# Performance work log

Hardware: AMD Instinct MI355X
Metric: run time of the kernel (lower is better)

## Reference

```python
import jax, jax.numpy as jnp
import numpy as np

F_DIM = 256; H = 4; LAT = 256; BOT = 128
B = 64; NPG = 180; N = B * NPG; E = N * 16; HF = H * F_DIM
NEG_SLOPE = 0.2  # PyG GATConv default LeakyReLU slope


def _gat(x, src, dst, W, att_s, att_d, bias):
    # PyG GATConv (concat=True): h = x W, per-edge score LeakyReLU(a_s[src]+a_d[dst]),
    # softmax over incoming edges of each dst, weighted sum, concat heads, + bias.
    h = (x @ W).reshape(N, H, F_DIM)
    a_s = jnp.einsum('nhc,hc->nh', h, att_s)
    a_d = jnp.einsum('nhc,hc->nh', h, att_d)
    e = jax.nn.leaky_relu(a_s[src] + a_d[dst], NEG_SLOPE)          # [E+N, H]
    m = jax.ops.segment_max(e, dst, num_segments=N)                # stable softmax per dst
    p = jnp.exp(e - m[dst])
    s = jax.ops.segment_sum(p, dst, num_segments=N)
    alpha = p / (s[dst] + 1e-16)
    out = jax.ops.segment_sum(alpha[:, :, None] * h[src], dst, num_segments=N)
    return out.reshape(N, HF) + bias


def setup_inputs() -> dict:
    key = jax.random.key(0)
    ks = jax.random.split(key, 40)
    def rn(i, shape, scale):
        return jax.random.normal(ks[i], shape, jnp.float32) * jnp.float32(scale)
    inp = {}
    inp['z'] = jax.random.normal(ks[0], (B, LAT), jnp.float32)
    inp['condition'] = jax.random.normal(ks[1], (B, BOT), jnp.float32)
    dst = jax.random.randint(ks[2], (E,), 0, N)
    off = jax.random.randint(ks[3], (E,), 1, NPG)
    src = (dst + off) % N  # no self-loops by construction (PyG adds them itself)
    inp['edge_index'] = jnp.stack([src, dst]).astype(jnp.int32)
    inp['batch'] = jnp.repeat(jnp.arange(B, dtype=jnp.int32), NPG)
    def lin(i, fin, fout):
        s = 1.0 / np.sqrt(fin)
        return rn(i, (fin, fout), s), rn(i + 1, (fout,), s)
    inp['W_init'], inp['b_init'] = lin(4, LAT + BOT, F_DIM)
    inp['W1'] = rn(6, (F_DIM + 180, HF), 1.0 / np.sqrt(F_DIM + 180))
    inp['as1'] = rn(7, (H, F_DIM), 0.1); inp['ad1'] = rn(8, (H, F_DIM), 0.1)
    inp['b1'] = rn(9, (HF,), 0.1)
    inp['W2'] = rn(10, (HF, HF), 1.0 / np.sqrt(HF))
    inp['as2'] = rn(11, (H, F_DIM), 0.1); inp['ad2'] = rn(12, (H, F_DIM), 0.1)
    inp['b2'] = rn(13, (HF,), 0.1)
    inp['W3'] = rn(14, (HF, HF), 1.0 / np.sqrt(HF))
    inp['as3'] = rn(15, (H, F_DIM), 0.1); inp['ad3'] = rn(16, (H, F_DIM), 0.1)
    inp['b3'] = rn(17, (HF,), 0.1)
    inp['Wp'], inp['bp'] = lin(18, HF, F_DIM)
    inp['Wfp'], inp['bfp'] = lin(20, F_DIM, 2)
    inp['Ws'], inp['bs'] = lin(22, HF, F_DIM)
    inp['Wfs'], inp['bfs'] = lin(24, F_DIM, 2)
    inp['Wt'], inp['bt'] = lin(26, HF, F_DIM)
    inp['Wft'], inp['bft'] = lin(28, F_DIM, 1)
    return inp


def reference(z, condition, edge_index, batch, W_init, b_init,
              W1, as1, ad1, b1, W2, as2, ad2, b2, W3, as3, ad3, b3,
              Wp, bp, Wfp, bfp, Ws, bs, Wfs, bfs, Wt, bt, Wft, bft):
    zc = jnp.concatenate([z, condition], axis=1) @ W_init + b_init  # [B, F]
    x = zc[batch]                                                    # [N, F]
    # node order within each (sorted) batch segment -> one-hot(180)
    start = jnp.searchsorted(batch, jnp.arange(B, dtype=batch.dtype))
    order = jnp.arange(N) - start[batch]
    pos = jax.nn.one_hot(order, 180, dtype=x.dtype)
    x = jax.nn.relu(jnp.concatenate([x, pos], axis=1))               # [N, F+180]
    # add self loops (PyG GATConv default add_self_loops=True)
    loops = jnp.arange(N, dtype=edge_index.dtype)
    src = jnp.concatenate([edge_index[0], loops])
    dst = jnp.concatenate([edge_index[1], loops])
    x = jax.nn.relu(_gat(x, src, dst, W1, as1, ad1, b1))
    x = jax.nn.relu(_gat(x, src, dst, W2, as2, ad2, b2))
    x = jax.nn.relu(_gat(x, src, dst, W3, as3, ad3, b3))
    out_pos = jax.nn.relu(x @ Wp + bp) @ Wfp + bfp     # [N, 2]
    out_size = jax.nn.relu(x @ Ws + bs) @ Wfs + bfs    # [N, 2]
    out_theta = jax.nn.relu(x @ Wt + bt) @ Wft + bft   # [N, 1]
    return out_pos, out_size, out_theta
```

## Files before the change

### kernel.cpp

```cpp
#include <hip/hip_runtime.h>
#include <hip/hip_bf16.h>

#define NODES 11520
#define EDGES 184320
#define NB    64
#define NPG   180
#define CAP   64

typedef __bf16 bf16x8 __attribute__((ext_vector_type(8)));
typedef __bf16 bf16x4 __attribute__((ext_vector_type(4)));
typedef float  f32x4  __attribute__((ext_vector_type(4)));

__global__ __launch_bounds__(256) void k_init(
    const float* __restrict__ z, const float* __restrict__ cond,
    const float* __restrict__ Wi, const float* __restrict__ bi,
    const float* __restrict__ W1, float* __restrict__ Y1)
{
    __shared__ float xr[384];
    __shared__ float zr[256];
    const int b = blockIdx.x, t = threadIdx.x;
    xr[t] = z[b * 256 + t];
    if (t < 128) xr[256 + t] = cond[b * 128 + t];
    __syncthreads();
    float acc = bi[t];
#pragma unroll 4
    for (int k = 0; k < 384; ++k) acc = fmaf(xr[k], Wi[k * 256 + t], acc);
    zr[t] = fmaxf(acc, 0.f);
    __syncthreads();
    float a0 = 0, a1 = 0, a2 = 0, a3 = 0;
#pragma unroll 4
    for (int k = 0; k < 256; ++k) {
        const float x = zr[k];
        const float* w = W1 + (size_t)k * 1024 + t;
        a0 = fmaf(x, w[0],   a0);
        a1 = fmaf(x, w[256], a1);
        a2 = fmaf(x, w[512], a2);
        a3 = fmaf(x, w[768], a3);
    }
    float* y = Y1 + (size_t)b * 1024 + t;
    y[0] = a0; y[256] = a1; y[512] = a2; y[768] = a3;
}

__global__ __launch_bounds__(256) void k_h1(
    const float* __restrict__ Y1, const float* __restrict__ W1,
    const float* __restrict__ atts, const float* __restrict__ attd,
    __bf16* __restrict__ hb, float* __restrict__ asb, float* __restrict__ adb)
{
    const int n = blockIdx.x, t = threadIdx.x;
    const int g = n / NPG, o = n - g * NPG;
    const float4 y = *(const float4*)(Y1 + (size_t)g * 1024 + 4 * t);
    const float4 w = *(const float4*)(W1 + (size_t)(256 + o) * 1024 + 4 * t);
    const float4 h = {y.x + w.x, y.y + w.y, y.z + w.z, y.w + w.w};
    bf16x4 hv = {(__bf16)h.x, (__bf16)h.y, (__bf16)h.z, (__bf16)h.w};
    *(bf16x4*)(hb + (size_t)n * 1024 + 4 * t) = hv;
    const int head = t >> 6, c0 = (t & 63) * 4;
    const float4 s4 = *(const float4*)(atts + head * 256 + c0);
    const float4 d4 = *(const float4*)(attd + head * 256 + c0);
    float ps = h.x * s4.x + h.y * s4.y + h.z * s4.z + h.w * s4.w;
    float pd = h.x * d4.x + h.y * d4.y + h.z * d4.z + h.w * d4.w;
    for (int off = 32; off; off >>= 1) {
        ps += __shfl_xor(ps, off, 64);
        pd += __shfl_xor(pd, off, 64);
    }
    if ((t & 63) == 0) { asb[n * 4 + head] = ps; adb[n * 4 + head] = pd; }
}

__global__ __launch_bounds__(256) void k_hist(
    const int* __restrict__ ei, int* __restrict__ counts,
    int* __restrict__ bucket)
{
    const int e = blockIdx.x * 256 + threadIdx.x;
    if (e >= EDGES) return;
    const int s = ei[e], d = ei[EDGES + e];
    const int pos = atomicAdd(&counts[d], 1);
    if (pos < CAP) bucket[(size_t)d * CAP + pos] = s;
}

__global__ __launch_bounds__(256) void k_agg(
    const __bf16* __restrict__ hb, const float* __restrict__ asb,
    const float* __restrict__ adb, const int* __restrict__ counts,
    const int* __restrict__ bucket, const float* __restrict__ bias,
    __bf16* __restrict__ xout)
{
    const int l = blockIdx.x;
    const int n = (l & 7) * (NODES / 8) + (l >> 3);
    const int t = threadIdx.x;
    __shared__ float sc[CAP + 1][4];
    __shared__ int   ssrc[CAP + 1];
    __shared__ float sinv[4];
    const int deg = min(counts[n], CAP);
    const int ne  = deg + 1;
    if (t < deg)       ssrc[t] = bucket[(size_t)n * CAP + t];
    else if (t == deg) ssrc[t] = n;
    __syncthreads();
    if (t < ne) {
        const int s = ssrc[t];
        const float4 as4 = *(const float4*)(asb + (size_t)s * 4);
        const float4 ad4 = *(const float4*)(adb + (size_t)n * 4);
        const float v0 = as4.x + ad4.x, v1 = as4.y + ad4.y;
        const float v2 = as4.z + ad4.z, v3 = as4.w + ad4.w;
        sc[t][0] = v0 > 0.f ? v0 : 0.2f * v0;
        sc[t][1] = v1 > 0.f ? v1 : 0.2f * v1;
        sc[t][2] = v2 > 0.f ? v2 : 0.2f * v2;
        sc[t][3] = v3 > 0.f ? v3 : 0.2f * v3;
    }
    __syncthreads();
    const int wv = t >> 6, ln = t & 63;
    {
        float m = -1e30f;
        for (int k = ln; k < ne; k += 64) m = fmaxf(m, sc[k][wv]);
        for (int off = 32; off; off >>= 1) m = fmaxf(m, __shfl_xor(m, off, 64));
        float s = 0.f;
        for (int k = ln; k < ne; k += 64) {
            const float p = __expf(sc[k][wv] - m);
            sc[k][wv] = p;
            s += p;
        }
        for (int off = 32; off; off >>= 1) s += __shfl_xor(s, off, 64);
        if (ln == 0) sinv[wv] = 1.f / (s + 1e-16f);
    }
    __syncthreads();
    const int j0 = t * 4;
    const float inv = sinv[wv];
    float a0 = 0, a1 = 0, a2 = 0, a3 = 0;
    int k = 0;
    for (; k + 4 <= ne; k += 4) {
        float al[4]; bf16x4 hv[4];
#pragma unroll
        for (int u = 0; u < 4; ++u) {
            al[u] = sc[k + u][wv] * inv;
            hv[u] = *(const bf16x4*)(hb + (size_t)ssrc[k + u] * 1024 + j0);
        }
#pragma unroll
        for (int u = 0; u < 4; ++u) {
            a0 = fmaf(al[u], (float)hv[u][0], a0);
            a1 = fmaf(al[u], (float)hv[u][1], a1);
            a2 = fmaf(al[u], (float)hv[u][2], a2);
            a3 = fmaf(al[u], (float)hv[u][3], a3);
        }
    }
    for (; k < ne; ++k) {
        const float al = sc[k][wv] * inv;
        const bf16x4 hv = *(const bf16x4*)(hb + (size_t)ssrc[k] * 1024 + j0);
        a0 = fmaf(al, (float)hv[0], a0);
        a1 = fmaf(al, (float)hv[1], a1);
        a2 = fmaf(al, (float)hv[2], a2);
        a3 = fmaf(al, (float)hv[3], a3);
    }
    const float4 b4 = *(const float4*)(bias + j0);
    bf16x4 o = {(__bf16)fmaxf(a0 + b4.x, 0.f), (__bf16)fmaxf(a1 + b4.y, 0.f),
                (__bf16)fmaxf(a2 + b4.z, 0.f), (__bf16)fmaxf(a3 + b4.w, 0.f)};
    *(bf16x4*)(xout + (size_t)n * 1024 + j0) = o;
}

__global__ __launch_bounds__(256) void k_transW(
    const float* __restrict__ W2, const float* __restrict__ W3,
    __bf16* __restrict__ W2t, __bf16* __restrict__ W3t)
{
    const float* W = blockIdx.z ? W3 : W2;
    __bf16* WT = blockIdx.z ? W3t : W2t;
    __shared__ float t[32][33];
    const int n0 = blockIdx.x * 32, k0 = blockIdx.y * 32;
    const int tx = threadIdx.x & 31, ty = threadIdx.x >> 5;
#pragma unroll
    for (int i = 0; i < 32; i += 8)
        t[ty + i][tx] = W[(size_t)(k0 + ty + i) * 1024 + n0 + tx];
    __syncthreads();
#pragma unroll
    for (int i = 0; i < 32; i += 8)
        WT[(size_t)(n0 + ty + i) * 1024 + k0 + tx] = (__bf16)t[tx][ty + i];
}

__global__ __launch_bounds__(256) void k_transH(
    const float* __restrict__ Wp, const float* __restrict__ Ws,
    const float* __restrict__ Wt, __bf16* __restrict__ WHt,
    const float* __restrict__ bp, const float* __restrict__ bs,
    const float* __restrict__ bt, float* __restrict__ bc)
{
    if (blockIdx.x == 8) {
        if (blockIdx.y == 0) {
            const int t = blockIdx.z * 256 + threadIdx.x;
            const float v = blockIdx.z == 0 ? bp[threadIdx.x]
                          : blockIdx.z == 1 ? bs[threadIdx.x] : bt[threadIdx.x];
            bc[t] = v;
        }
        return;
    }
    const float* W = blockIdx.z == 0 ? Wp : blockIdx.z == 1 ? Ws : Wt;
    __bf16* WT = WHt + (size_t)blockIdx.z * 256 * 1024;
    __shared__ float t[32][33];
    const int n0 = blockIdx.x * 32, k0 = blockIdx.y * 32;
    const int tx = threadIdx.x & 31, ty = threadIdx.x >> 5;
#pragma unroll
    for (int i = 0; i < 32; i += 8)
        t[ty + i][tx] = W[(size_t)(k0 + ty + i) * 256 + n0 + tx];
    __syncthreads();
#pragma unroll
    for (int i = 0; i < 32; i += 8)
        WT[(size_t)(n0 + ty + i) * 1024 + k0 + tx] = (__bf16)t[tx][ty + i];
}

__global__ __launch_bounds__(256) void gemm_bf16_h(
    const __bf16* __restrict__ A,
    const __bf16* __restrict__ BT,
    __bf16* __restrict__ Cb,
    const float* __restrict__ atts, const float* __restrict__ attd,
    float* __restrict__ asb, float* __restrict__ adb,
    int M, int N, int K)
{
    const int lb = blockIdx.x;
    const int g = lb & 7, idx = lb >> 3;
    const int bx = idx & 7;
    const int by = (idx >> 3) * 8 + g;
    if (by * 128 >= M) return;
    const int m0 = by * 128, n0 = bx * 128;

    __shared__ __bf16 As[128 * 32];
    __shared__ __bf16 Bs[128 * 32];
    const int tid = threadIdx.x;
    const int w = tid >> 6, l = tid & 63;
    const int lr = l >> 2;
    const int lk = (l & 3) * 8;
    const int quad = l >> 4, r16 = l & 15;
    const int wm = (w >> 1) * 64, wn = (w & 1) * 64;

    f32x4 acc[4][4];
#pragma unroll
    for (int i = 0; i < 4; ++i)
#pragma unroll
        for (int j = 0; j < 4; ++j)
            acc[i][j] = (f32x4){0.f, 0.f, 0.f, 0.f};

    for (int k0 = 0; k0 < K; k0 += 32) {
#pragma unroll
        for (int cc = 0; cc < 2; ++cc) {
            const int c = 2 * w + cc;
            const int row = c * 16 + lr;
            __builtin_amdgcn_global_load_lds(
                (const __attribute__((address_space(1))) void*)
                    (A + (size_t)(m0 + row) * K + k0 + lk),
                (__attribute__((address_space(3))) void*)(As + c * 512),
                16, 0, 0);
            __builtin_amdgcn_global_load_lds(
                (const __attribute__((address_space(1))) void*)
                    (BT + (size_t)(n0 + row) * K + k0 + lk),
                (__attribute__((address_space(3))) void*)(Bs + c * 512),
                16, 0, 0);
        }
        __syncthreads();
        bf16x8 af[4], bfr[4];
#pragma unroll
        for (int i = 0; i < 4; ++i)
            af[i] = *(const bf16x8*)(As + (wm + i * 16 + r16) * 32 + quad * 8);
#pragma unroll
        for (int j = 0; j < 4; ++j)
            bfr[j] = *(const bf16x8*)(Bs + (wn + j * 16 + r16) * 32 + quad * 8);
#pragma unroll
        for (int i = 0; i < 4; ++i)
#pragma unroll
            for (int j = 0; j < 4; ++j)
                acc[i][j] = __builtin_amdgcn_mfma_f32_16x16x32_bf16(
                    af[i], bfr[j], acc[i][j], 0, 0, 0);
        __syncthreads();
    }
    const int head = (n0 + wn) >> 8;
    const float* Sa = atts + head * 256;
    const float* Da = attd + head * 256;
#pragma unroll
    for (int i = 0; i < 4; ++i) {
#pragma unroll
        for (int r = 0; r < 4; ++r) {
            const int mg = m0 + wm + i * 16 + quad * 4 + r;
            float ps = 0.f, pd = 0.f;
#pragma unroll
            for (int j = 0; j < 4; ++j) {
                const int ng = n0 + wn + j * 16 + r16;
                const float v = acc[i][j][r];
                const int cl = ng & 255;
                ps = fmaf(v, Sa[cl], ps);
                pd = fmaf(v, Da[cl], pd);
                Cb[(size_t)mg * N + ng] = (__bf16)v;
            }
            for (int off = 8; off; off >>= 1) {
                ps += __shfl_xor(ps, off, 64);
                pd += __shfl_xor(pd, off, 64);
            }
            if (r16 == 0) {
                atomicAdd(&asb[mg * 4 + head], ps);
                atomicAdd(&adb[mg * 4 + head], pd);
            }
        }
    }
}

__global__ __launch_bounds__(256) void gemm_bf16_f32(
    const __bf16* __restrict__ A, const __bf16* __restrict__ BT,
    float* __restrict__ C, const float* __restrict__ bias,
    int M, int N, int K)
{
    const int lb = blockIdx.x;
    const int g = lb & 7, idx = lb >> 3;
    const int bx = idx % 6;
    const int by = (idx / 6) * 8 + g;
    if (by * 128 >= M) return;
    const int m0 = by * 128, n0 = bx * 128;

    __shared__ __bf16 As[128 * 32];
    __shared__ __bf16 Bs[128 * 32];
    const int tid = threadIdx.x;
    const int w = tid >> 6, l = tid & 63;
    const int lr = l >> 2;
    const int lk = (l & 3) * 8;
    const int quad = l >> 4, r16 = l & 15;
    const int wm = (w >> 1) * 64, wn = (w & 1) * 64;

    f32x4 acc[4][4];
#pragma unroll
    for (int i = 0; i < 4; ++i)
#pragma unroll
        for (int j = 0; j < 4; ++j)
            acc[i][j] = (f32x4){0.f, 0.f, 0.f, 0.f};

    for (int k0 = 0; k0 < K; k0 += 32) {
#pragma unroll
        for (int cc = 0; cc < 2; ++cc) {
            const int c = 2 * w + cc;
            const int row = c * 16 + lr;
            __builtin_amdgcn_global_load_lds(
                (const __attribute__((address_space(1))) void*)
                    (A + (size_t)(m0 + row) * K + k0 + lk),
                (__attribute__((address_space(3))) void*)(As + c * 512),
                16, 0, 0);
            __builtin_amdgcn_global_load_lds(
                (const __attribute__((address_space(1))) void*)
                    (BT + (size_t)(n0 + row) * K + k0 + lk),
                (__attribute__((address_space(3))) void*)(Bs + c * 512),
                16, 0, 0);
        }
        __syncthreads();
        bf16x8 af[4], bfr[4];
#pragma unroll
        for (int i = 0; i < 4; ++i)
            af[i] = *(const bf16x8*)(As + (wm + i * 16 + r16) * 32 + quad * 8);
#pragma unroll
        for (int j = 0; j < 4; ++j)
            bfr[j] = *(const bf16x8*)(Bs + (wn + j * 16 + r16) * 32 + quad * 8);
#pragma unroll
        for (int i = 0; i < 4; ++i)
#pragma unroll
            for (int j = 0; j < 4; ++j)
                acc[i][j] = __builtin_amdgcn_mfma_f32_16x16x32_bf16(
                    af[i], bfr[j], acc[i][j], 0, 0, 0);
        __syncthreads();
    }
#pragma unroll
    for (int i = 0; i < 4; ++i) {
        const int mg = m0 + wm + i * 16 + quad * 4;
#pragma unroll
        for (int j = 0; j < 4; ++j) {
            const int ng = n0 + wn + j * 16 + r16;
            const float bz = bias[ng];
#pragma unroll
            for (int r = 0; r < 4; ++r)
                C[(size_t)(mg + r) * N + ng] = fmaxf(acc[i][j][r] + bz, 0.f);
        }
    }
}

__global__ __launch_bounds__(320) void k_final(
    const float* __restrict__ T,
    const float* __restrict__ Wfp, const float* __restrict__ bfp,
    const float* __restrict__ Wfs, const float* __restrict__ bfs,
    const float* __restrict__ Wft, const float* __restrict__ bft,
    float* __restrict__ out)
{
    const int n = blockIdx.x;
    const int w = threadIdx.x >> 6, l = threadIdx.x & 63;
    const float* trow;
    const float* Wf;
    float bv;
    int col, stride, oidx;
    if (w < 2) {
        trow = T + (size_t)n * 768;       Wf = Wfp; bv = bfp[w];
        col = w; stride = 2; oidx = 2 * n + w;
    } else if (w < 4) {
        trow = T + (size_t)n * 768 + 256; Wf = Wfs; bv = bfs[w - 2];
        col = w - 2; stride = 2; oidx = 2 * NODES + 2 * n + (w - 2);
    } else {
        trow = T + (size_t)n * 768 + 512; Wf = Wft; bv = bft[0];
        col = 0; stride = 1; oidx = 4 * NODES + n;
    }
    float s = 0.f;
    for (int c = l; c < 256; c += 64) s = fmaf(trow[c], Wf[c * stride + col], s);
    for (int off = 32; off; off >>= 1) s += __shfl_xor(s, off, 64);
    if (l == 0) out[oidx] = s + bv;
}

extern "C" void kernel_launch(void* const* d_in, const int* in_sizes, int n_in,
                              void* d_out, int out_size, void* d_ws, size_t ws_size,
                              hipStream_t stream)
{
    const float* z    = (const float*)d_in[0];
    const float* cond = (const float*)d_in[1];
    const int*   ei   = (const int*)  d_in[2];
    const float* Wi   = (const float*)d_in[4];
    const float* bi   = (const float*)d_in[5];
    const float* W1   = (const float*)d_in[6];
    const float* as1  = (const float*)d_in[7];
    const float* ad1  = (const float*)d_in[8];
    const float* b1   = (const float*)d_in[9];
    const float* W2   = (const float*)d_in[10];
    const float* as2  = (const float*)d_in[11];
    const float* ad2  = (const float*)d_in[12];
    const float* b2   = (const float*)d_in[13];
    const float* W3   = (const float*)d_in[14];
    const float* as3  = (const float*)d_in[15];
    const float* ad3  = (const float*)d_in[16];
    const float* b3   = (const float*)d_in[17];
    const float* Wp   = (const float*)d_in[18];
    const float* bp   = (const float*)d_in[19];
    const float* Wfp  = (const float*)d_in[20];
    const float* bfp  = (const float*)d_in[21];
    const float* Ws   = (const float*)d_in[22];
    const float* bs   = (const float*)d_in[23];
    const float* Wfs  = (const float*)d_in[24];
    const float* bfs  = (const float*)d_in[25];
    const float* Wt   = (const float*)d_in[26];
    const float* bt   = (const float*)d_in[27];
    const float* Wft  = (const float*)d_in[28];
    const float* bft  = (const float*)d_in[29];
    float* out = (float*)d_out;

    char* p = (char*)d_ws;
    __bf16* hb    = (__bf16*)p;           p += (size_t)NODES * 1024 * 2;
    __bf16* xb16  = (__bf16*)p;           p += (size_t)NODES * 1024 * 2;
    float* Tbuf   = (float*)p;            p += (size_t)NODES * 768 * 4;
    float* asb    = (float*)p;            p += (size_t)NODES * 4 * 4;
    float* adb    = (float*)p;            p += (size_t)NODES * 4 * 4;
    float* Y1     = (float*)p;            p += 64 * 1024 * 4;
    int*   counts = (int*)p;              p += (size_t)NODES * 4;
    int*   bucket = (int*)p;              p += (size_t)NODES * CAP * 4;
    __bf16* W2t   = (__bf16*)p;           p += (size_t)1024 * 1024 * 2;
    __bf16* W3t   = (__bf16*)p;           p += (size_t)1024 * 1024 * 2;
    __bf16* WHt   = (__bf16*)p;           p += (size_t)768 * 1024 * 2;
    float* biascat= (float*)p;            p += 768 * 4;

    k_transW<<<dim3(32, 32, 2), 256, 0, stream>>>(W2, W3, W2t, W3t);
    k_transH<<<dim3(9, 32, 3), 256, 0, stream>>>(Wp, Ws, Wt, WHt,
                                                 bp, bs, bt, biascat);

    hipMemsetAsync(counts, 0, NODES * sizeof(int), stream);
    k_hist<<<EDGES / 256, 256, 0, stream>>>(ei, counts, bucket);

    k_init<<<NB, 256, 0, stream>>>(z, cond, Wi, bi, W1, Y1);
    k_h1<<<NODES, 256, 0, stream>>>(Y1, W1, as1, ad1, hb, asb, adb);
    k_agg<<<NODES, 256, 0, stream>>>(hb, asb, adb, counts, bucket, b1, xb16);

    hipMemsetAsync(asb, 0, (size_t)NODES * 8 * sizeof(float), stream);
    gemm_bf16_h<<<8 * 96, 256, 0, stream>>>(xb16, W2t, hb, as2, ad2,
                                            asb, adb, NODES, 1024, 1024);
    k_agg<<<NODES, 256, 0, stream>>>(hb, asb, adb, counts, bucket, b2, xb16);

    hipMemsetAsync(asb, 0, (size_t)NODES * 8 * sizeof(float), stream);
    gemm_bf16_h<<<8 * 96, 256, 0, stream>>>(xb16, W3t, hb, as3, ad3,
                                            asb, adb, NODES, 1024, 1024);
    k_agg<<<NODES, 256, 0, stream>>>(hb, asb, adb, counts, bucket, b3, xb16);

    gemm_bf16_f32<<<6 * 96, 256, 0, stream>>>(xb16, WHt, Tbuf, biascat,
                                              NODES, 768, 1024);
    k_final<<<NODES, 320, 0, stream>>>(Tbuf, Wfp, bfp, Wfs, bfs, Wft, bft, out);
}
```

Measured before the change: 463.4 us.

## Widen GEMM K-step to 64 and vectorize/split init MLP matvecs

Both bf16 MFMA GEMMs now load two 32-wide K slices per iteration into doubled LDS buffers. This halves the number of barrier pairs and gives each load phase more memory requests in flight. The init kernel now splits the 384-long first matvec across four wave groups, which reduce partial sums through LDS. Both init matvecs use float4 weight loads. The costs are more LDS per block, which may lower occupancy, and extra reduction work in the init kernel.

Result: faster. 445.3 us (-3.9%).

```diff
diff --git a/kernel.cpp b/kernel.cpp
--- a/kernel.cpp
+++ b/kernel.cpp
@@ -17,28 +17,44 @@
     const float* __restrict__ W1, float* __restrict__ Y1)
 {
     __shared__ float xr[384];
+    __shared__ float part[4][256];
     __shared__ float zr[256];
     const int b = blockIdx.x, t = threadIdx.x;
-    xr[t] = z[b * 256 + t];
+    xr[t] = (t < 256) ? z[b * 256 + t] : 0.f;
     if (t < 128) xr[256 + t] = cond[b * 128 + t];
     __syncthreads();
-    float acc = bi[t];
-#pragma unroll 4
-    for (int k = 0; k < 384; ++k) acc = fmaf(xr[k], Wi[k * 256 + t], acc);
-    zr[t] = fmaxf(acc, 0.f);
-    __syncthreads();
-    float a0 = 0, a1 = 0, a2 = 0, a3 = 0;
-#pragma unroll 4
-    for (int k = 0; k < 256; ++k) {
-        const float x = zr[k];
-        const float* w = W1 + (size_t)k * 1024 + t;
-        a0 = fmaf(x, w[0],   a0);
-        a1 = fmaf(x, w[256], a1);
-        a2 = fmaf(x, w[512], a2);
-        a3 = fmaf(x, w[768], a3);
-    }
-    float* y = Y1 + (size_t)b * 1024 + t;
-    y[0] = a0; y[256] = a1; y[512] = a2; y[768] = a3;
+    {
+        const int kq = t >> 6, tc = t & 63;
+        f32x4 acc = {0.f, 0.f, 0.f, 0.f};
+        const float* wbase = Wi + (size_t)(kq * 96) * 256 + 4 * tc;
+        const float* xb = xr + kq * 96;
+#pragma unroll 8
+        for (int k = 0; k < 96; ++k) {
+            const float4 w = *(const float4*)(wbase + (size_t)k * 256);
+            const float x = xb[k];
+            acc[0] = fmaf(x, w.x, acc[0]);
+            acc[1] = fmaf(x, w.y, acc[1]);
+            acc[2] = fmaf(x, w.z, acc[2]);
+            acc[3] = fmaf(x, w.w, acc[3]);
+        }
+        *(f32x4*)&part[kq][4 * tc] = acc;
+    }
+    __syncthreads();
+    zr[t] = fmaxf(bi[t] + part[0][t] + part[1][t] + part[2][t] + part[3][t], 0.f);
+    __syncthreads();
+    {
+        f32x4 acc = {0.f, 0.f, 0.f, 0.f};
+#pragma unroll 8
+        for (int k = 0; k < 256; ++k) {
+            const float4 w = *(const float4*)(W1 + (size_t)k * 1024 + 4 * t);
+            const float x = zr[k];
+            acc[0] = fmaf(x, w.x, acc[0]);
+            acc[1] = fmaf(x, w.y, acc[1]);
+            acc[2] = fmaf(x, w.z, acc[2]);
+            acc[3] = fmaf(x, w.w, acc[3]);
+        }
+        *(f32x4*)(Y1 + (size_t)b * 1024 + 4 * t) = acc;
+    }
 }
 
 __global__ __launch_bounds__(256) void k_h1(
@@ -215,8 +231,8 @@
     if (by * 128 >= M) return;
     const int m0 = by * 128, n0 = bx * 128;
 
-    __shared__ __bf16 As[128 * 32];
-    __shared__ __bf16 Bs[128 * 32];
+    __shared__ __bf16 As[2 * 128 * 32];
+    __shared__ __bf16 Bs[2 * 128 * 32];
     const int tid = threadIdx.x;
     const int w = tid >> 6, l = tid & 63;
     const int lr = l >> 2;
@@ -231,36 +247,46 @@
         for (int j = 0; j < 4; ++j)
             acc[i][j] = (f32x4){0.f, 0.f, 0.f, 0.f};
 
-    for (int k0 = 0; k0 < K; k0 += 32) {
-#pragma unroll
-        for (int cc = 0; cc < 2; ++cc) {
-            const int c = 2 * w + cc;
-            const int row = c * 16 + lr;
-            __builtin_amdgcn_global_load_lds(
-                (const __attribute__((address_space(1))) void*)
-                    (A + (size_t)(m0 + row) * K + k0 + lk),
-                (__attribute__((address_space(3))) void*)(As + c * 512),
-                16, 0, 0);
-            __builtin_amdgcn_global_load_lds(
-                (const __attribute__((address_space(1))) void*)
-                    (BT + (size_t)(n0 + row) * K + k0 + lk),
-                (__attribute__((address_space(3))) void*)(Bs + c * 512),
-                16, 0, 0);
+    for (int k0 = 0; k0 < K; k0 += 64) {
+#pragma unroll
+        for (int h = 0; h < 2; ++h) {
+#pragma unroll
+            for (int cc = 0; cc < 2; ++cc) {
+                const int c = 2 * w + cc;
+                const int row = c * 16 + lr;
+                __builtin_amdgcn_global_load_lds(
+                    (const __attribute__((address_space(1))) void*)
+                        (A + (size_t)(m0 + row) * K + k0 + h * 32 + lk),
+                    (__attribute__((address_space(3))) void*)
+                        (As + h * 4096 + c * 512),
+                    16, 0, 0);
+                __builtin_amdgcn_global_load_lds(
+                    (const __attribute__((address_space(1))) void*)
+                        (BT + (size_t)(n0 + row) * K + k0 + h * 32 + lk),
+                    (__attribute__((address_space(3))) void*)
+                        (Bs + h * 4096 + c * 512),
+                    16, 0, 0);
+            }
         }
         __syncthreads();
-        bf16x8 af[4], bfr[4];
-#pragma unroll
-        for (int i = 0; i < 4; ++i)
-            af[i] = *(const bf16x8*)(As + (wm + i * 16 + r16) * 32 + quad * 8);
-#pragma unroll
-        for (int j = 0; j < 4; ++j)
-            bfr[j] = *(const bf16x8*)(Bs + (wn + j * 16 + r16) * 32 + quad * 8);
-#pragma unroll
-        for (int i = 0; i < 4; ++i)
+#pragma unroll
+        for (int h = 0; h < 2; ++h) {
+            bf16x8 af[4], bfr[4];
+#pragma unroll
+            for (int i = 0; i < 4; ++i)
+                af[i] = *(const bf16x8*)(As + h * 4096 +
+                                         (wm + i * 16 + r16) * 32 + quad * 8);
 #pragma unroll
             for (int j = 0; j < 4; ++j)
-                acc[i][j] = __builtin_amdgcn_mfma_f32_16x16x32_bf16(
-                    af[i], bfr[j], acc[i][j], 0, 0, 0);
+                bfr[j] = *(const bf16x8*)(Bs + h * 4096 +
+                                          (wn + j * 16 + r16) * 32 + quad * 8);
+#pragma unroll
+            for (int i = 0; i < 4; ++i)
+#pragma unroll
+                for (int j = 0; j < 4; ++j)
+                    acc[i][j] = __builtin_amdgcn_mfma_f32_16x16x32_bf16(
+                        af[i], bfr[j], acc[i][j], 0, 0, 0);
+        }
         __syncthreads();
     }
     const int head = (n0 + wn) >> 8;
@@ -305,8 +331,8 @@
     if (by * 128 >= M) return;
     const int m0 = by * 128, n0 = bx * 128;
 
-    __shared__ __bf16 As[128 * 32];
-    __shared__ __bf16 Bs[128 * 32];
+    __shared__ __bf16 As[2 * 128 * 32];
+    __shared__ __bf16 Bs[2 * 128 * 32];
     const int tid = threadIdx.x;
     const int w = tid >> 6, l = tid & 63;
     const int lr = l >> 2;
@@ -321,36 +347,46 @@
         for (int j = 0; j < 4; ++j)
             acc[i][j] = (f32x4){0.f, 0.f, 0.f, 0.f};
 
-    for (int k0 = 0; k0 < K; k0 += 32) {
-#pragma unroll
-        for (int cc = 0; cc < 2; ++cc) {
-            const int c = 2 * w + cc;
-            const int row = c * 16 + lr;
-            __builtin_amdgcn_global_load_lds(
-                (const __attribute__((address_space(1))) void*)
-                    (A + (size_t)(m0 + row) * K + k0 + lk),
-                (__attribute__((address_space(3))) void*)(As + c * 512),
-                16, 0, 0);
-            __builtin_amdgcn_global_load_lds(
-                (const __attribute__((address_space(1))) void*)
-                    (BT + (size_t)(n0 + row) * K + k0 + lk),
-                (__attribute__((address_space(3))) void*)(Bs + c * 512),
-                16, 0, 0);
+    for (int k0 = 0; k0 < K; k0 += 64) {
+#pragma unroll
+        for (int h = 0; h < 2; ++h) {
+#pragma unroll
+            for (int cc = 0; cc < 2; ++cc) {
+                const int c = 2 * w + cc;
+                const int row = c * 16 + lr;
+                __builtin_amdgcn_global_load_lds(
+                    (const __attribute__((address_space(1))) void*)
+                        (A + (size_t)(m0 + row) * K + k0 + h * 32 + lk),
+                    (__attribute__((address_space(3))) void*)
+                        (As + h * 4096 + c * 512),
+                    16, 0, 0);
+                __builtin_amdgcn_global_load_lds(
+                    (const __attribute__((address_space(1))) void*)
+                        (BT + (size_t)(n0 + row) * K + k0 + h * 32 + lk),
+                    (__attribute__((address_space(3))) void*)
+                        (Bs + h * 4096 + c * 512),
+                    16, 0, 0);
+            }
         }
         __syncthreads();
-        bf16x8 af[4], bfr[4];
-#pragma unroll
-        for (int i = 0; i < 4; ++i)
-            af[i] = *(const bf16x8*)(As + (wm + i * 16 + r16) * 32 + quad * 8);
-#pragma unroll
-        for (int j = 0; j < 4; ++j)
-            bfr[j] = *(const bf16x8*)(Bs + (wn + j * 16 + r16) * 32 + quad * 8);
-#pragma unroll
-        for (int i = 0; i < 4; ++i)
+#pragma unroll
+        for (int h = 0; h < 2; ++h) {
+            bf16x8 af[4], bfr[4];
+#pragma unroll
+            for (int i = 0; i < 4; ++i)
+                af[i] = *(const bf16x8*)(As + h * 4096 +
+                                         (wm + i * 16 + r16) * 32 + quad * 8);
 #pragma unroll
             for (int j = 0; j < 4; ++j)
-                acc[i][j] = __builtin_amdgcn_mfma_f32_16x16x32_bf16(
-                    af[i], bfr[j], acc[i][j], 0, 0, 0);
+                bfr[j] = *(const bf16x8*)(Bs + h * 4096 +
+                                          (wn + j * 16 + r16) * 32 + quad * 8);
+#pragma unroll
+            for (int i = 0; i < 4; ++i)
+#pragma unroll
+                for (int j = 0; j < 4; ++j)
+                    acc[i][j] = __builtin_amdgcn_mfma_f32_16x16x32_bf16(
+                        af[i], bfr[j], acc[i][j], 0, 0, 0);
+        }
         __syncthreads();
     }
 #pragma unroll
```
